# Kernel optimization log

Hardware: AMD Instinct MI355X
Metric: run time of the kernel (lower is better)

The kernel has to match this reference:

```python
import jax, jax.numpy as jnp
import numpy as np
from jax import lax

B, T_ENC, T_DEC = 32, 256, 256
N_MEL = 80
MEM_D = 768
ATT_RNN = 1024
DEC_RNN = 1024
PRENET = 256
ATT_D = 128
NF = 32
K = 31
PAD = (K - 1) // 2


def setup_inputs() -> dict:
    key = jax.random.key(0)
    ks = jax.random.split(key, 20)
    def w(k, shape, fan_in):
        return jax.random.normal(k, shape, jnp.float32) / np.sqrt(fan_in).astype(np.float32)
    inp = {}
    inp['memory'] = jax.random.normal(ks[0], (B, T_ENC, MEM_D), jnp.float32)
    inp['decoder_inputs'] = jax.random.normal(ks[1], (T_DEC, B, N_MEL), jnp.float32)
    inp['mask'] = jnp.zeros((B, T_ENC), bool)
    inp['prenet_W1'] = w(ks[2], (PRENET, N_MEL), N_MEL)
    inp['prenet_W2'] = w(ks[3], (PRENET, PRENET), PRENET)
    att_in = PRENET + MEM_D
    inp['att_Wih'] = w(ks[4], (4 * ATT_RNN, att_in), att_in)
    inp['att_Whh'] = w(ks[5], (4 * ATT_RNN, ATT_RNN), ATT_RNN)
    inp['att_bih'] = jnp.zeros((4 * ATT_RNN,), jnp.float32)
    inp['att_bhh'] = jnp.zeros((4 * ATT_RNN,), jnp.float32)
    inp['query_W'] = w(ks[6], (ATT_D, ATT_RNN), ATT_RNN)
    inp['memory_W'] = w(ks[7], (ATT_D, MEM_D), MEM_D)
    inp['v_W'] = w(ks[8], (1, ATT_D), ATT_D)
    inp['loc_conv_W'] = w(ks[9], (NF, 2, K), 2 * K)
    inp['loc_dense_W'] = w(ks[10], (ATT_D, NF), NF)
    dec_in = ATT_RNN + MEM_D
    inp['dec_Wih'] = w(ks[11], (4 * DEC_RNN, dec_in), dec_in)
    inp['dec_Whh'] = w(ks[12], (4 * DEC_RNN, DEC_RNN), DEC_RNN)
    inp['dec_bih'] = jnp.zeros((4 * DEC_RNN,), jnp.float32)
    inp['dec_bhh'] = jnp.zeros((4 * DEC_RNN,), jnp.float32)
    proj_in = DEC_RNN + MEM_D
    inp['proj_W'] = w(ks[13], (N_MEL, proj_in), proj_in)
    inp['proj_b'] = jnp.zeros((N_MEL,), jnp.float32)
    inp['gate_W'] = w(ks[14], (1, proj_in), proj_in)
    inp['gate_b'] = jnp.zeros((1,), jnp.float32)
    return inp


def _lstm_cell(x, h, c, Wih, Whh, bih, bhh):
    gates = x @ Wih.T + h @ Whh.T + (bih + bhh)
    i, f, g, o = jnp.split(gates, 4, axis=-1)
    c2 = jax.nn.sigmoid(f) * c + jax.nn.sigmoid(i) * jnp.tanh(g)
    h2 = jax.nn.sigmoid(o) * jnp.tanh(c2)
    return h2, c2


def _decode(memory, decoder_inputs, mask, prenet_W1, prenet_W2,
            att_Wih, att_Whh, att_bih, att_bhh,
            query_W, memory_W, v_W, loc_conv_W, loc_dense_W,
            dec_Wih, dec_Whh, dec_bih, dec_bhh,
            proj_W, proj_b, gate_W, gate_b):
    # teacher forcing: inputs are [go_frame, target[:-1]]
    go = jnp.zeros((1, B, N_MEL), decoder_inputs.dtype)
    x = jnp.concatenate([go, decoder_inputs[:-1]], axis=0)  # [T_DEC, B, N_MEL]
    # prenet (no dropout, p=0): two relu linears, bias=False
    x = jax.nn.relu(x @ prenet_W1.T)
    x = jax.nn.relu(x @ prenet_W2.T)  # [T_DEC, B, PRENET]
    processed_memory = memory @ memory_W.T  # [B, T_ENC, ATT_D]
    v = v_W[0]  # [ATT_D]

    def step(carry, x_t):
        att_h, att_c, dec_h, dec_c, aw, aw_cum, ctx = carry
        cell_in = jnp.concatenate([x_t, ctx], axis=-1)
        att_h, att_c = _lstm_cell(cell_in, att_h, att_c, att_Wih, att_Whh, att_bih, att_bhh)
        # location-sensitive attention
        awc = jnp.stack([aw, aw_cum], axis=1)  # [B, 2, T_ENC]
        loc = lax.conv_general_dilated(awc, loc_conv_W, window_strides=(1,),
                                       padding=[(PAD, PAD)],
                                       dimension_numbers=('NCH', 'OIH', 'NCH'))  # [B, NF, T_ENC]
        processed = jnp.einsum('bft,af->bta', loc, loc_dense_W)  # [B, T_ENC, ATT_D]
        query = att_h @ query_W.T  # [B, ATT_D]
        energies = jnp.einsum('bta,a->bt', jnp.tanh(processed + query[:, None, :] + processed_memory), v)
        energies = jnp.where(mask, -jnp.inf, energies)
        aw = jax.nn.softmax(energies, axis=1)  # [B, T_ENC]
        ctx = jnp.einsum('bt,btd->bd', aw, memory)  # [B, MEM_D]
        aw_cum = aw_cum + aw
        dec_in = jnp.concatenate([att_h, ctx], axis=-1)
        dec_h, dec_c = _lstm_cell(dec_in, dec_h, dec_c, dec_Wih, dec_Whh, dec_bih, dec_bhh)
        proj_in = jnp.concatenate([dec_h, ctx], axis=-1)
        mel = proj_in @ proj_W.T + proj_b  # [B, N_MEL]
        gate = (proj_in @ gate_W.T + gate_b)[:, 0]  # [B]
        return (att_h, att_c, dec_h, dec_c, aw, aw_cum, ctx), (mel, gate, aw)

    f32 = memory.dtype
    carry0 = (jnp.zeros((B, ATT_RNN), f32), jnp.zeros((B, ATT_RNN), f32),
              jnp.zeros((B, DEC_RNN), f32), jnp.zeros((B, DEC_RNN), f32),
              jnp.zeros((B, T_ENC), f32), jnp.zeros((B, T_ENC), f32),
              jnp.zeros((B, MEM_D), f32))
    _, (mels, gates, aligns) = lax.scan(step, carry0, x)
    # [B, T_DEC, N_MEL], [B, T_DEC], [B, T_DEC, T_ENC]
    return mels.transpose(1, 0, 2), gates.T, aligns.transpose(1, 0, 2)


def reference(memory, decoder_inputs, mask, prenet_W1, prenet_W2,
              att_Wih, att_Whh, att_bih, att_bhh,
              query_W, memory_W, v_W, loc_conv_W, loc_dense_W,
              dec_Wih, dec_Whh, dec_bih, dec_bhh,
              proj_W, proj_b, gate_W, gate_b):
    return _decode(memory, decoder_inputs, mask, prenet_W1, prenet_W2,
                   att_Wih, att_Whh, att_bih, att_bhh,
                   query_W, memory_W, v_W, loc_conv_W, loc_dense_W,
                   dec_Wih, dec_Whh, dec_bih, dec_bhh,
                   proj_W, proj_b, gate_W, gate_b)
```

## Files before the change

### kernel.cpp

```cpp
#include <hip/hip_runtime.h>
#include <cstddef>

#define TB   32
#define TENC 256
#define TDEC 256
#define NMEL 80
#define MEMD 768
#define ARNN 1024
#define PRN  256
#define ATTD 128
#define NFLT 32
#define KSZ  31
#define KPAD 15
#define SSTR 260
#define NAB  128
#define NEB  256
#define NCB  128
#define NATT 32

__device__ __forceinline__ float sigf(float x){ return 1.f/(1.f+expf(-x)); }

__global__ __launch_bounds__(256) void k_prenet1(const float* __restrict__ din,
                                                 const float* __restrict__ W1,
                                                 float* __restrict__ out){
  const int row = blockIdx.x;
  const int t = row >> 5, b = row & 31;
  const int tid = threadIdx.x;
  __shared__ float x[NMEL];
  if (tid < NMEL) x[tid] = (t == 0) ? 0.f : din[((size_t)(t-1)*TB + b)*NMEL + tid];
  __syncthreads();
  const float* wr = W1 + (size_t)tid*NMEL;
  float s = 0.f;
  #pragma unroll
  for (int m = 0; m < NMEL; ++m) s += x[m]*wr[m];
  out[(size_t)row*PRN + tid] = fmaxf(s, 0.f);
}

__global__ __launch_bounds__(256) void k_prenet2(float* __restrict__ buf,
                                                 const float* __restrict__ W2){
  const int row = blockIdx.x;
  const int tid = threadIdx.x;
  __shared__ float x[PRN];
  x[tid] = buf[(size_t)row*PRN + tid];
  __syncthreads();
  const float4* wr = (const float4*)(W2 + (size_t)tid*PRN);
  const float4* xx = (const float4*)x;
  float s = 0.f;
  #pragma unroll 8
  for (int k = 0; k < PRN/4; ++k) {
    float4 w = wr[k], v = xx[k];
    s += w.x*v.x + w.y*v.y + w.z*v.z + w.w*v.w;
  }
  buf[(size_t)row*PRN + tid] = fmaxf(s, 0.f);
}

__global__ __launch_bounds__(128) void k_procmem(const float* __restrict__ mem,
                                                 const float* __restrict__ mW,
                                                 float* __restrict__ pm){
  const int row = blockIdx.x;
  const int tid = threadIdx.x;
  __shared__ float x[MEMD];
  for (int i = tid; i < MEMD; i += 128) x[i] = mem[(size_t)row*MEMD + i];
  __syncthreads();
  const float4* wr = (const float4*)(mW + (size_t)tid*MEMD);
  const float4* xx = (const float4*)x;
  float s = 0.f;
  #pragma unroll 8
  for (int k = 0; k < MEMD/4; ++k) {
    float4 w = wr[k], v = xx[k];
    s += w.x*v.x + w.y*v.y + w.z*v.z + w.w*v.w;
  }
  pm[(size_t)row*ATTD + tid] = s;
}

__device__ __forceinline__ void lstm_body(int bi, int tid,
    float* smem, float* ldsg,
    const float* __restrict__ in1, int L1,
    const float* __restrict__ in2, int L2,
    const float* __restrict__ hbm,
    const float* __restrict__ Wih, const float* __restrict__ Whh,
    const float* __restrict__ bih, const float* __restrict__ bhh,
    const float* __restrict__ cT_in, float* cT_out, float* h_bm_out)
{
  const int Kin = L1 + L2, Ktot = Kin + ARNN;
  const int w = tid >> 6, lane = tid & 63;
  const int r = lane >> 4, kl = lane & 15;
  const int up = w >> 1, bh = w & 1, b0 = bh*16;
  const int j0 = bi*8 + up*4;
  float acc[4][16];
  #pragma unroll
  for (int u = 0; u < 4; ++u)
    #pragma unroll
    for (int b = 0; b < 16; ++b) acc[u][b] = 0.f;

  for (int kc = 0; kc < Ktot; kc += 256) {
    const float* src; int kq, Ls;
    if (kc < L1)       { src = in1; kq = kc;       Ls = L1; }
    else if (kc < Kin) { src = in2; kq = kc - L1;  Ls = L2; }
    else               { src = hbm; kq = kc - Kin; Ls = ARNN; }
    const float* Wb; int rs, kof;
    if (kc < Kin) { Wb = Wih; rs = Kin;  kof = kc; }
    else          { Wb = Whh; rs = ARNN; kof = kc - Kin; }
    float4 wv[4][4];
    {
      const float* wr0 = Wb + (size_t)(r*ARNN + j0)*rs + kof;
      #pragma unroll
      for (int u = 0; u < 4; ++u) {
        const float* wru = wr0 + (size_t)u*rs;
        wv[u][0] = *(const float4*)(wru + (0*16 + kl)*4);
        wv[u][1] = *(const float4*)(wru + (1*16 + kl)*4);
        wv[u][2] = *(const float4*)(wru + (2*16 + kl)*4);
        wv[u][3] = *(const float4*)(wru + (3*16 + kl)*4);
      }
    }
    __syncthreads();
    #pragma unroll
    for (int tc = 0; tc < 8; ++tc) {
      const int f4 = tid + tc*256;
      const int bb = f4 >> 6, k4 = f4 & 63;
      *(float4*)(&smem[bb*SSTR + k4*4]) =
          *(const float4*)(src + (size_t)bb*Ls + kq + k4*4);
    }
    __syncthreads();
    #pragma unroll
    for (int b = 0; b < 16; ++b) {
      const float* sb = &smem[(b0 + b)*SSTR + kl*4];
      const float4 s0 = *(const float4*)(sb + 0*64);
      const float4 s1 = *(const float4*)(sb + 1*64);
      const float4 s2 = *(const float4*)(sb + 2*64);
      const float4 s3 = *(const float4*)(sb + 3*64);
      #pragma unroll
      for (int u = 0; u < 4; ++u) {
        float a = acc[u][b];
        a = fmaf(wv[u][0].x,s0.x, fmaf(wv[u][0].y,s0.y, fmaf(wv[u][0].z,s0.z, fmaf(wv[u][0].w,s0.w, a))));
        a = fmaf(wv[u][1].x,s1.x, fmaf(wv[u][1].y,s1.y, fmaf(wv[u][1].z,s1.z, fmaf(wv[u][1].w,s1.w, a))));
        a = fmaf(wv[u][2].x,s2.x, fmaf(wv[u][2].y,s2.y, fmaf(wv[u][2].z,s2.z, fmaf(wv[u][2].w,s2.w, a))));
        a = fmaf(wv[u][3].x,s3.x, fmaf(wv[u][3].y,s3.y, fmaf(wv[u][3].z,s3.z, fmaf(wv[u][3].w,s3.w, a))));
        acc[u][b] = a;
      }
    }
  }
  #pragma unroll
  for (int u = 0; u < 4; ++u)
    #pragma unroll
    for (int b = 0; b < 16; ++b) {
      acc[u][b] += __shfl_xor(acc[u][b], 1);
      acc[u][b] += __shfl_xor(acc[u][b], 2);
      acc[u][b] += __shfl_xor(acc[u][b], 4);
      acc[u][b] += __shfl_xor(acc[u][b], 8);
    }
  if (kl == 0) {
    #pragma unroll
    for (int u = 0; u < 4; ++u)
      #pragma unroll
      for (int b = 0; b < 16; ++b)
        ldsg[((w*4 + u)*4 + r)*17 + b] = acc[u][b];
  }
  {
    const int u2 = lane >> 4, bl = lane & 15;
    const int b = b0 + bl, j = j0 + u2;
    const float gi = ldsg[((w*4 + u2)*4 + 0)*17 + bl] + bih[j]          + bhh[j];
    const float gf = ldsg[((w*4 + u2)*4 + 1)*17 + bl] + bih[ARNN + j]   + bhh[ARNN + j];
    const float gg = ldsg[((w*4 + u2)*4 + 2)*17 + bl] + bih[2*ARNN + j] + bhh[2*ARNN + j];
    const float go = ldsg[((w*4 + u2)*4 + 3)*17 + bl] + bih[3*ARNN + j] + bhh[3*ARNN + j];
    const float c  = sigf(gf)*cT_in[j*32 + b] + sigf(gi)*tanhf(gg);
    const float h  = sigf(go)*tanhf(c);
    cT_out[j*32 + b] = c;
    h_bm_out[(size_t)b*ARNN + j] = h;
  }
}

__device__ __forceinline__ void eterm_body(int eb, int tid, float* smem,
    const float* __restrict__ aw_prev, int awp_stride,
    const float* __restrict__ aw_cum,
    const float* __restrict__ conv_W, const float* __restrict__ dense_W,
    const float* __restrict__ pm, float* __restrict__ eterm)
{
  const int b   = eb >> 3;
  const int te0 = (eb & 7)*32;
  float* awp = smem;
  float* awc = smem + 64;
  float* cw  = smem + 128;
  float* loc = smem + 2112;
  if (tid < 62) {
    const int te = te0 - KPAD + tid;
    const bool ok = (te >= 0) && (te < TENC);
    awp[tid] = ok ? aw_prev[(size_t)b*awp_stride + te] : 0.f;
    awc[tid] = ok ? aw_cum[(size_t)b*TENC + te] : 0.f;
  }
  for (int i = tid; i < NFLT*2*KSZ; i += 256) cw[i] = conv_W[i];
  __syncthreads();
  {
    const int te = tid & 31;
    const int fq = tid >> 5;
    #pragma unroll
    for (int ff = 0; ff < 4; ++ff) {
      const int f = fq*4 + ff;
      const float* wf = cw + f*2*KSZ;
      float s = 0.f;
      #pragma unroll
      for (int kk = 0; kk < KSZ; ++kk) s += awp[te+kk]*wf[kk];
      #pragma unroll
      for (int kk = 0; kk < KSZ; ++kk) s += awc[te+kk]*wf[KSZ+kk];
      loc[f*33 + te] = s;
    }
  }
  __syncthreads();
  {
    const int a  = tid & 127;
    const int th = tid >> 7;
    float la[NFLT];
    const float* lr = dense_W + (size_t)a*NFLT;
    #pragma unroll
    for (int f = 0; f < NFLT; ++f) la[f] = lr[f];
    #pragma unroll
    for (int t4 = 0; t4 < 16; ++t4) {
      const int tel = th*16 + t4;
      const int te = te0 + tel;
      float accv = pm[((size_t)b*TENC + te)*ATTD + a];
      #pragma unroll 8
      for (int f = 0; f < NFLT; ++f) accv = fmaf(la[f], loc[f*33 + tel], accv);
      eterm[((size_t)b*TENC + te)*ATTD + a] = accv;
    }
  }
}

__device__ __forceinline__ void attn_body(int b, int tid, float* smem, int t,
    const float* __restrict__ att_h, const float* __restrict__ query_W,
    const float* __restrict__ v_W, const float* __restrict__ eterm,
    float* __restrict__ out_al, float* __restrict__ aw_cum,
    const float* __restrict__ mem, float* __restrict__ ctx_out)
{
  float* hrow = smem;
  float* qp   = smem + 1024;
  float* q    = smem + 1280;
  float* vv   = smem + 1408;
  float* aws  = smem + 1536;
  float* red  = smem + 1792;
  ((float4*)hrow)[tid] = ((const float4*)(att_h + (size_t)b*ARNN))[tid];
  if (tid < ATTD) vv[tid] = v_W[tid];
  __syncthreads();
  {
    const int a = tid & 127, kh = tid >> 7;
    const float4* wr = (const float4*)(query_W + (size_t)a*ARNN + kh*512);
    const float4* xx = (const float4*)(hrow + kh*512);
    float s = 0.f;
    #pragma unroll 8
    for (int k = 0; k < 128; ++k) {
      float4 w = wr[k], x = xx[k];
      s += w.x*x.x + w.y*x.y + w.z*x.z + w.w*x.w;
    }
    qp[tid] = s;
  }
  __syncthreads();
  if (tid < ATTD) q[tid] = qp[tid] + qp[128 + tid];
  __syncthreads();
  float e = 0.f;
  {
    const float* etr = eterm + ((size_t)b*TENC + tid)*ATTD;
    #pragma unroll 8
    for (int a4 = 0; a4 < 32; ++a4) {
      float4 t4 = *(const float4*)(etr + a4*4);
      e += vv[a4*4+0]*tanhf(q[a4*4+0] + t4.x);
      e += vv[a4*4+1]*tanhf(q[a4*4+1] + t4.y);
      e += vv[a4*4+2]*tanhf(q[a4*4+2] + t4.z);
      e += vv[a4*4+3]*tanhf(q[a4*4+3] + t4.w);
    }
  }
  float m1 = e;
  #pragma unroll
  for (int d = 1; d < 64; d <<= 1) m1 = fmaxf(m1, __shfl_xor(m1, d, 64));
  if ((tid & 63) == 0) red[tid >> 6] = m1;
  __syncthreads();
  const float mx = fmaxf(fmaxf(red[0], red[1]), fmaxf(red[2], red[3]));
  const float p = expf(e - mx);
  float s1 = p;
  #pragma unroll
  for (int d = 1; d < 64; d <<= 1) s1 += __shfl_xor(s1, d, 64);
  if ((tid & 63) == 0) red[4 + (tid >> 6)] = s1;
  __syncthreads();
  const float sden = red[4] + red[5] + red[6] + red[7];
  const float aw = p / sden;
  out_al[(size_t)b*TDEC*TENC + (size_t)t*TENC + tid] = aw;
  aw_cum[(size_t)b*TENC + tid] += aw;
  aws[tid] = aw;
  __syncthreads();
  if (tid < 192) {
    const float* mc = mem + (size_t)b*TENC*MEMD + tid*4;
    float4 s4 = make_float4(0.f, 0.f, 0.f, 0.f);
    #pragma unroll 8
    for (int te = 0; te < 256; ++te) {
      float4 m4 = *(const float4*)(mc + (size_t)te*MEMD);
      const float a = aws[te];
      s4.x = fmaf(a, m4.x, s4.x); s4.y = fmaf(a, m4.y, s4.y);
      s4.z = fmaf(a, m4.z, s4.z); s4.w = fmaf(a, m4.w, s4.w);
    }
    *(float4*)(ctx_out + (size_t)b*MEMD + tid*4) = s4;
  }
}

__global__ __launch_bounds__(256, 2) void k_phase1(
    int tA, int ncb,
    float* cx, float* ahbm2, float* dhbm, float* dcT,
    const float* __restrict__ dWih, const float* __restrict__ dWhh,
    const float* __restrict__ dbih, const float* __restrict__ dbhh,
    float* out_al, float* awcum,
    const float* __restrict__ et,
    const float* __restrict__ qW, const float* __restrict__ vW,
    const float* __restrict__ mem)
{
  __shared__ float smem[32*SSTR];
  __shared__ float ldsg[4*4*4*17];
  int bi = blockIdx.x;
  const int tid = threadIdx.x;
  if (bi < ncb) {
    const int tD = tA - 1;
    const int curD = tD & 1, nxtD = curD ^ 1;
    lstm_body(bi, tid, smem, ldsg,
        ahbm2 + (size_t)nxtD*TB*ARNN, ARNN,
        cx + (size_t)(tD+1)*TB*MEMD, MEMD,
        dhbm + (size_t)tD*TB*ARNN,
        dWih, dWhh, dbih, dbhh,
        dcT + (size_t)curD*ARNN*TB, dcT + (size_t)nxtD*ARNN*TB,
        dhbm + (size_t)(tD+1)*TB*ARNN);
    return;
  }
  bi -= ncb;
  const int nxt = (tA & 1) ^ 1;
  attn_body(bi, tid, smem, tA,
      ahbm2 + (size_t)nxt*TB*ARNN, qW, vW, et,
      out_al, awcum, mem, cx + (size_t)(tA+1)*TB*MEMD);
}

__global__ __launch_bounds__(256, 2) void k_phase2(
    int tA, int nab,
    const float* __restrict__ xp, const float* __restrict__ cx,
    float* ahbm2, float* acT,
    const float* __restrict__ aWih, const float* __restrict__ aWhh,
    const float* __restrict__ abih, const float* __restrict__ abhh,
    const float* __restrict__ aw0, const float* __restrict__ out_al,
    const float* __restrict__ awcum,
    const float* __restrict__ cvW, const float* __restrict__ ldW,
    const float* __restrict__ pm, float* __restrict__ et)
{
  __shared__ float smem[32*SSTR];
  __shared__ float ldsg[4*4*4*17];
  int bi = blockIdx.x;
  const int tid = threadIdx.x;
  if (bi < nab) {
    const int cur = tA & 1, nxt = cur ^ 1;
    lstm_body(bi, tid, smem, ldsg,
        xp + (size_t)tA*TB*PRN, PRN,
        cx + (size_t)tA*TB*MEMD, MEMD,
        ahbm2 + (size_t)cur*TB*ARNN,
        aWih, aWhh, abih, abhh,
        acT + (size_t)cur*ARNN*TB, acT + (size_t)nxt*ARNN*TB,
        ahbm2 + (size_t)nxt*TB*ARNN);
    return;
  }
  bi -= nab;
  {
    const float* awprev = (tA == 0) ? aw0 : (out_al + (size_t)(tA-1)*TENC);
    const int awps = (tA == 0) ? TENC : TDEC*TENC;
    eterm_body(bi, tid, smem, awprev, awps, awcum, cvW, ldW, pm, et);
  }
}

__global__ __launch_bounds__(192) void k_proj(
    const float* __restrict__ dh_all,
    const float* __restrict__ cx_all,
    const float* __restrict__ proj_W,
    const float* __restrict__ proj_b,
    const float* __restrict__ gate_W,
    const float* __restrict__ gate_b,
    float* __restrict__ out_mel,
    float* __restrict__ out_gate)
{
  const int b = blockIdx.y;
  const int tid = threadIdx.x;
  __shared__ float pin[ARNN + MEMD];
  __shared__ float pp[192];
  for (int t0 = 0; t0 < 32; ++t0) {
    const int t = blockIdx.x*32 + t0;
    __syncthreads();
    for (int i = tid; i < 448; i += 192) {
      float4 v;
      if (i < 256) v = *(const float4*)(dh_all + ((size_t)(t+1)*TB + b)*ARNN + i*4);
      else         v = *(const float4*)(cx_all + ((size_t)(t+1)*TB + b)*MEMD + (i-256)*4);
      *(float4*)(&pin[i*4]) = v;
    }
    __syncthreads();
    if (tid < 160) {
      const int m = tid >> 1, kh = tid & 1;
      const float4* wr = (const float4*)(proj_W + (size_t)m*1792 + kh*896);
      const float4* xx = (const float4*)(pin + kh*896);
      float s = 0.f;
      #pragma unroll 8
      for (int k = 0; k < 224; ++k) {
        float4 w = wr[k], x = xx[k];
        s += w.x*x.x + w.y*x.y + w.z*x.z + w.w*x.w;
      }
      pp[tid] = s;
    } else if (tid == 160) {
      const float4* wr = (const float4*)gate_W;
      const float4* xx = (const float4*)pin;
      float s = 0.f;
      #pragma unroll 8
      for (int k = 0; k < 448; ++k) {
        float4 w = wr[k], x = xx[k];
        s += w.x*x.x + w.y*x.y + w.z*x.z + w.w*x.w;
      }
      out_gate[(size_t)b*TDEC + t] = s + gate_b[0];
    }
    __syncthreads();
    if (tid < NMEL) out_mel[((size_t)b*TDEC + t)*NMEL + tid] = pp[2*tid] + pp[2*tid+1] + proj_b[tid];
  }
}

extern "C" void kernel_launch(void* const* d_in, const int* in_sizes, int n_in,
                              void* d_out, int out_size, void* d_ws, size_t ws_size,
                              hipStream_t stream) {
  const float* mem  = (const float*)d_in[0];
  const float* din  = (const float*)d_in[1];
  const float* pW1  = (const float*)d_in[3];
  const float* pW2  = (const float*)d_in[4];
  const float* aWih = (const float*)d_in[5];
  const float* aWhh = (const float*)d_in[6];
  const float* abih = (const float*)d_in[7];
  const float* abhh = (const float*)d_in[8];
  const float* qW   = (const float*)d_in[9];
  const float* mW   = (const float*)d_in[10];
  const float* vW   = (const float*)d_in[11];
  const float* cvW  = (const float*)d_in[12];
  const float* ldW  = (const float*)d_in[13];
  const float* dWih = (const float*)d_in[14];
  const float* dWhh = (const float*)d_in[15];
  const float* dbih = (const float*)d_in[16];
  const float* dbhh = (const float*)d_in[17];
  const float* prW  = (const float*)d_in[18];
  const float* prb  = (const float*)d_in[19];
  const float* gW   = (const float*)d_in[20];
  const float* gb   = (const float*)d_in[21];

  float* ws = (float*)d_ws;
  size_t o = 0;
  float* xp    = ws + o; o += (size_t)TDEC*TB*PRN;
  float* pm    = ws + o; o += (size_t)TB*TENC*ATTD;
  float* et    = ws + o; o += (size_t)TB*TENC*ATTD;
  float* acT   = ws + o; o += (size_t)2*ARNN*TB;
  float* dcT   = ws + o; o += (size_t)2*ARNN*TB;
  float* ahbm2 = ws + o; o += (size_t)2*TB*ARNN;
  float* dhbm  = ws + o; o += (size_t)(TDEC+1)*TB*ARNN;
  float* cx    = ws + o; o += (size_t)(TDEC+2)*TB*MEMD;
  float* awcum = ws + o; o += (size_t)TB*TENC;
  float* aw0   = ws + o; o += (size_t)TB*TENC;
  if (ws_size < o*sizeof(float)) return;

  float* out_mel  = (float*)d_out;
  float* out_gate = out_mel + (size_t)TB*TDEC*NMEL;
  float* out_al   = out_gate + (size_t)TB*TDEC;

  (void)hipMemsetAsync(acT, 0, (size_t)2*ARNN*TB*sizeof(float), stream);
  (void)hipMemsetAsync(dcT, 0, (size_t)2*ARNN*TB*sizeof(float), stream);
  (void)hipMemsetAsync(ahbm2, 0, (size_t)2*TB*ARNN*sizeof(float), stream);
  (void)hipMemsetAsync(dhbm, 0, (size_t)TB*ARNN*sizeof(float), stream);
  (void)hipMemsetAsync(cx, 0, (size_t)TB*MEMD*sizeof(float), stream);
  (void)hipMemsetAsync(awcum, 0, (size_t)TB*TENC*sizeof(float), stream);
  (void)hipMemsetAsync(aw0, 0, (size_t)TB*TENC*sizeof(float), stream);

  k_prenet1<<<TDEC*TB, 256, 0, stream>>>(din, pW1, xp);
  k_prenet2<<<TDEC*TB, 256, 0, stream>>>(xp, pW2);
  k_procmem<<<TB*TENC, 128, 0, stream>>>(mem, mW, pm);

  k_phase2<<<NAB + NEB, 256, 0, stream>>>(
      0, NAB, xp, cx, ahbm2, acT,
      aWih, aWhh, abih, abhh,
      aw0, out_al, awcum, cvW, ldW, pm, et);

  for (int t = 0; t < TDEC; ++t) {
    const int ncb = (t > 0) ? NCB : 0;
    k_phase1<<<ncb + NATT, 256, 0, stream>>>(
        t, ncb, cx, ahbm2, dhbm, dcT,
        dWih, dWhh, dbih, dbhh,
        out_al, awcum, et, qW, vW, mem);
    if (t < TDEC - 1) {
      k_phase2<<<NAB + NEB, 256, 0, stream>>>(
          t + 1, NAB, xp, cx, ahbm2, acT,
          aWih, aWhh, abih, abhh,
          aw0, out_al, awcum, cvW, ldW, pm, et);
    }
  }
  k_phase1<<<NCB, 256, 0, stream>>>(
      TDEC, NCB, cx, ahbm2, dhbm, dcT,
      dWih, dWhh, dbih, dbhh,
      out_al, awcum, et, qW, vW, mem);

  k_proj<<<dim3(8, TB), 192, 0, stream>>>(dhbm, cx, prW, prb, gW, gb, out_mel, out_gate);
}
```

Before: 21.58 ms.

## Split LSTM gate GEMVs into partial sums computed alongside attention

Each LSTM's gate computation is split into two parts. The parts that depend only on already-available hidden states (att Whh·h, and dec Wih·att_h plus dec Whh·dec_h) are computed into global partial-gate buffers in the same launch as attention. The remaining context- and prenet-dependent parts are finished in the next launch. This moves weight-streaming work off the serial critical path and balances the two per-step launches, at the cost of extra global round-trips for the partial gates and a more intricate dependency schedule.

```diff
diff --git a/kernel.cpp b/kernel.cpp
--- a/kernel.cpp
+++ b/kernel.cpp
@@ -13,9 +13,8 @@
 #define KSZ  31
 #define KPAD 15
 #define SSTR 260
-#define NAB  128
+#define NAF  128
 #define NEB  256
-#define NCB  128
 #define NATT 32
 
 __device__ __forceinline__ float sigf(float x){ return 1.f/(1.f+expf(-x)); }
@@ -73,16 +72,71 @@
   pm[(size_t)row*ATTD + tid] = s;
 }
 
-__device__ __forceinline__ void lstm_body(int bi, int tid,
-    float* smem, float* ldsg,
-    const float* __restrict__ in1, int L1,
-    const float* __restrict__ in2, int L2,
-    const float* __restrict__ hbm,
-    const float* __restrict__ Wih, const float* __restrict__ Whh,
-    const float* __restrict__ bih, const float* __restrict__ bhh,
-    const float* __restrict__ cT_in, float* cT_out, float* h_bm_out)
-{
-  const int Kin = L1 + L2, Ktot = Kin + ARNN;
+__device__ __forceinline__ void lstm_chunk(int tid, int r, int kl, int b0, int j0,
+    float* smem, const float* src, int Ls, int kq,
+    const float* W, int rs, int kof, float acc[4][16])
+{
+  float4 wv[4][4];
+  {
+    const float* wr0 = W + (size_t)(r*ARNN + j0)*rs + kof + kq;
+    #pragma unroll
+    for (int u = 0; u < 4; ++u) {
+      const float* wru = wr0 + (size_t)u*rs;
+      wv[u][0] = *(const float4*)(wru + (0*16 + kl)*4);
+      wv[u][1] = *(const float4*)(wru + (1*16 + kl)*4);
+      wv[u][2] = *(const float4*)(wru + (2*16 + kl)*4);
+      wv[u][3] = *(const float4*)(wru + (3*16 + kl)*4);
+    }
+  }
+  __syncthreads();
+  #pragma unroll
+  for (int tc = 0; tc < 8; ++tc) {
+    const int f4 = tid + tc*256;
+    const int bb = f4 >> 6, k4 = f4 & 63;
+    *(float4*)(&smem[bb*SSTR + k4*4]) =
+        *(const float4*)(src + (size_t)bb*Ls + kq + k4*4);
+  }
+  __syncthreads();
+  #pragma unroll
+  for (int b = 0; b < 16; ++b) {
+    const float* sb = &smem[(b0 + b)*SSTR + kl*4];
+    const float4 s0 = *(const float4*)(sb + 0*64);
+    const float4 s1 = *(const float4*)(sb + 1*64);
+    const float4 s2 = *(const float4*)(sb + 2*64);
+    const float4 s3 = *(const float4*)(sb + 3*64);
+    #pragma unroll
+    for (int u = 0; u < 4; ++u) {
+      float a = acc[u][b];
+      a = fmaf(wv[u][0].x,s0.x, fmaf(wv[u][0].y,s0.y, fmaf(wv[u][0].z,s0.z, fmaf(wv[u][0].w,s0.w, a))));
+      a = fmaf(wv[u][1].x,s1.x, fmaf(wv[u][1].y,s1.y, fmaf(wv[u][1].z,s1.z, fmaf(wv[u][1].w,s1.w, a))));
+      a = fmaf(wv[u][2].x,s2.x, fmaf(wv[u][2].y,s2.y, fmaf(wv[u][2].z,s2.z, fmaf(wv[u][2].w,s2.w, a))));
+      a = fmaf(wv[u][3].x,s3.x, fmaf(wv[u][3].y,s3.y, fmaf(wv[u][3].z,s3.z, fmaf(wv[u][3].w,s3.w, a))));
+      acc[u][b] = a;
+    }
+  }
+}
+
+__device__ __forceinline__ void lstm_reduce(int kl, int w, float* ldsg, float acc[4][16])
+{
+  #pragma unroll
+  for (int u = 0; u < 4; ++u)
+    #pragma unroll
+    for (int b = 0; b < 16; ++b) {
+      acc[u][b] += __shfl_xor(acc[u][b], 1);
+      acc[u][b] += __shfl_xor(acc[u][b], 2);
+      acc[u][b] += __shfl_xor(acc[u][b], 4);
+      acc[u][b] += __shfl_xor(acc[u][b], 8);
+    }
+  if (kl == 0) {
+    const int r = 0; (void)r;
+  }
+}
+
+__device__ __forceinline__ void lstm_part1(int bi, int tid, float* smem, float* ldsg,
+    const float* srcA, int LsA, const float* WA, int rsA, int kofA, int nchA,
+    const float* srcB, int LsB, const float* WB, int rsB, int kofB, int nchB,
+    float* __restrict__ gpart)
+{
   const int w = tid >> 6, lane = tid & 63;
   const int r = lane >> 4, kl = lane & 15;
   const int up = w >> 1, bh = w & 1, b0 = bh*16;
@@ -92,18 +146,59 @@
   for (int u = 0; u < 4; ++u)
     #pragma unroll
     for (int b = 0; b < 16; ++b) acc[u][b] = 0.f;
-
+  for (int c = 0; c < nchA; ++c)
+    lstm_chunk(tid, r, kl, b0, j0, smem, srcA, LsA, c*256, WA, rsA, kofA, acc);
+  for (int c = 0; c < nchB; ++c)
+    lstm_chunk(tid, r, kl, b0, j0, smem, srcB, LsB, c*256, WB, rsB, kofB, acc);
+  #pragma unroll
+  for (int u = 0; u < 4; ++u)
+    #pragma unroll
+    for (int b = 0; b < 16; ++b) {
+      acc[u][b] += __shfl_xor(acc[u][b], 1);
+      acc[u][b] += __shfl_xor(acc[u][b], 2);
+      acc[u][b] += __shfl_xor(acc[u][b], 4);
+      acc[u][b] += __shfl_xor(acc[u][b], 8);
+    }
+  if (kl == 0) {
+    #pragma unroll
+    for (int u = 0; u < 4; ++u)
+      #pragma unroll
+      for (int b = 0; b < 16; ++b)
+        ldsg[((w*4 + u)*4 + r)*17 + b] = acc[u][b];
+  }
+  __syncthreads();
+  for (int i = tid; i < 1024; i += 256) {
+    const int rr = i >> 8, u8 = (i >> 5) & 7, b = i & 31;
+    const int upp = u8 >> 2, uu = u8 & 3, bh2 = b >> 4, bl2 = b & 15;
+    gpart[(size_t)(rr*ARNN + bi*8 + u8)*32 + b] =
+        ldsg[(((upp*2 + bh2)*4 + uu)*4 + rr)*17 + bl2];
+  }
+}
+
+__device__ __forceinline__ void lstm_part2(int bi, int tid, float* smem, float* ldsg,
+    const float* in1, int L1, const float* in2, int L2,
+    const float* W, int rs, int kofBase,
+    const float* __restrict__ gpart,
+    const float* __restrict__ bih, const float* __restrict__ bhh,
+    const float* __restrict__ cT_in, float* cT_out, float* h_bm_out)
+{
+  const int w = tid >> 6, lane = tid & 63;
+  const int r = lane >> 4, kl = lane & 15;
+  const int up = w >> 1, bh = w & 1, b0 = bh*16;
+  const int j0 = bi*8 + up*4;
+  const int Ktot = L1 + L2;
+  float acc[4][16];
+  #pragma unroll
+  for (int u = 0; u < 4; ++u)
+    #pragma unroll
+    for (int b = 0; b < 16; ++b) acc[u][b] = 0.f;
   for (int kc = 0; kc < Ktot; kc += 256) {
     const float* src; int kq, Ls;
-    if (kc < L1)       { src = in1; kq = kc;       Ls = L1; }
-    else if (kc < Kin) { src = in2; kq = kc - L1;  Ls = L2; }
-    else               { src = hbm; kq = kc - Kin; Ls = ARNN; }
-    const float* Wb; int rs, kof;
-    if (kc < Kin) { Wb = Wih; rs = Kin;  kof = kc; }
-    else          { Wb = Whh; rs = ARNN; kof = kc - Kin; }
+    if (kc < L1) { src = in1; kq = kc;      Ls = L1; }
+    else         { src = in2; kq = kc - L1; Ls = L2; }
     float4 wv[4][4];
     {
-      const float* wr0 = Wb + (size_t)(r*ARNN + j0)*rs + kof;
+      const float* wr0 = W + (size_t)(r*ARNN + j0)*rs + kofBase + kc;
       #pragma unroll
       for (int u = 0; u < 4; ++u) {
         const float* wru = wr0 + (size_t)u*rs;
@@ -159,10 +254,14 @@
   {
     const int u2 = lane >> 4, bl = lane & 15;
     const int b = b0 + bl, j = j0 + u2;
-    const float gi = ldsg[((w*4 + u2)*4 + 0)*17 + bl] + bih[j]          + bhh[j];
-    const float gf = ldsg[((w*4 + u2)*4 + 1)*17 + bl] + bih[ARNN + j]   + bhh[ARNN + j];
-    const float gg = ldsg[((w*4 + u2)*4 + 2)*17 + bl] + bih[2*ARNN + j] + bhh[2*ARNN + j];
-    const float go = ldsg[((w*4 + u2)*4 + 3)*17 + bl] + bih[3*ARNN + j] + bhh[3*ARNN + j];
+    const float g0 = ldsg[((w*4 + u2)*4 + 0)*17 + bl] + gpart[(size_t)(0*ARNN + j)*32 + b];
+    const float g1 = ldsg[((w*4 + u2)*4 + 1)*17 + bl] + gpart[(size_t)(1*ARNN + j)*32 + b];
+    const float g2 = ldsg[((w*4 + u2)*4 + 2)*17 + bl] + gpart[(size_t)(2*ARNN + j)*32 + b];
+    const float g3 = ldsg[((w*4 + u2)*4 + 3)*17 + bl] + gpart[(size_t)(3*ARNN + j)*32 + b];
+    const float gi = g0 + bih[j]          + bhh[j];
+    const float gf = g1 + bih[ARNN + j]   + bhh[ARNN + j];
+    const float gg = g2 + bih[2*ARNN + j] + bhh[2*ARNN + j];
+    const float go = g3 + bih[3*ARNN + j] + bhh[3*ARNN + j];
     const float c  = sigf(gf)*cT_in[j*32 + b] + sigf(gi)*tanhf(gg);
     const float h  = sigf(go)*tanhf(c);
     cT_out[j*32 + b] = c;
@@ -299,45 +398,51 @@
   }
 }
 
-__global__ __launch_bounds__(256, 2) void k_phase1(
-    int tA, int ncb,
-    float* cx, float* ahbm2, float* dhbm, float* dcT,
-    const float* __restrict__ dWih, const float* __restrict__ dWhh,
-    const float* __restrict__ dbih, const float* __restrict__ dbhh,
+__global__ __launch_bounds__(256, 2) void k_lb(
+    int t,
+    const float* __restrict__ ahbm, float* cx,
     float* out_al, float* awcum,
     const float* __restrict__ et,
     const float* __restrict__ qW, const float* __restrict__ vW,
-    const float* __restrict__ mem)
+    const float* __restrict__ mem,
+    const float* __restrict__ aWhh,
+    const float* __restrict__ dWih, const float* __restrict__ dWhh,
+    const float* __restrict__ dhbm_t,
+    float* __restrict__ gpartA, float* __restrict__ gpartC)
 {
   __shared__ float smem[32*SSTR];
   __shared__ float ldsg[4*4*4*17];
   int bi = blockIdx.x;
   const int tid = threadIdx.x;
-  if (bi < ncb) {
-    const int tD = tA - 1;
-    const int curD = tD & 1, nxtD = curD ^ 1;
-    lstm_body(bi, tid, smem, ldsg,
-        ahbm2 + (size_t)nxtD*TB*ARNN, ARNN,
-        cx + (size_t)(tD+1)*TB*MEMD, MEMD,
-        dhbm + (size_t)tD*TB*ARNN,
-        dWih, dWhh, dbih, dbhh,
-        dcT + (size_t)curD*ARNN*TB, dcT + (size_t)nxtD*ARNN*TB,
-        dhbm + (size_t)(tD+1)*TB*ARNN);
+  if (bi < NATT) {
+    attn_body(bi, tid, smem, t, ahbm, qW, vW, et,
+        out_al, awcum, mem, cx + (size_t)(t+1)*TB*MEMD);
     return;
   }
-  bi -= ncb;
-  const int nxt = (tA & 1) ^ 1;
-  attn_body(bi, tid, smem, tA,
-      ahbm2 + (size_t)nxt*TB*ARNN, qW, vW, et,
-      out_al, awcum, mem, cx + (size_t)(tA+1)*TB*MEMD);
-}
-
-__global__ __launch_bounds__(256, 2) void k_phase2(
-    int tA, int nab,
-    const float* __restrict__ xp, const float* __restrict__ cx,
-    float* ahbm2, float* acT,
-    const float* __restrict__ aWih, const float* __restrict__ aWhh,
+  bi -= NATT;
+  if (bi < NAF) {
+    lstm_part1(bi, tid, smem, ldsg,
+        ahbm, ARNN, aWhh, ARNN, 0, 4,
+        nullptr, 0, nullptr, 0, 0, 0,
+        gpartA);
+    return;
+  }
+  bi -= NAF;
+  lstm_part1(bi, tid, smem, ldsg,
+      ahbm, ARNN, dWih, 1792, 0, 4,
+      dhbm_t, ARNN, dWhh, ARNN, 0, 4,
+      gpartC);
+}
+
+__global__ __launch_bounds__(256, 2) void k_la(
+    int t, int naf, int neb,
+    const float* __restrict__ xp, float* cx,
+    float* ahbm, float* acT, float* dhbm, float* dcT,
+    const float* __restrict__ aWih,
     const float* __restrict__ abih, const float* __restrict__ abhh,
+    const float* __restrict__ dWih,
+    const float* __restrict__ dbih, const float* __restrict__ dbhh,
+    const float* __restrict__ gpartA, const float* __restrict__ gpartC,
     const float* __restrict__ aw0, const float* __restrict__ out_al,
     const float* __restrict__ awcum,
     const float* __restrict__ cvW, const float* __restrict__ ldW,
@@ -347,22 +452,35 @@
   __shared__ float ldsg[4*4*4*17];
   int bi = blockIdx.x;
   const int tid = threadIdx.x;
-  if (bi < nab) {
-    const int cur = tA & 1, nxt = cur ^ 1;
-    lstm_body(bi, tid, smem, ldsg,
-        xp + (size_t)tA*TB*PRN, PRN,
-        cx + (size_t)tA*TB*MEMD, MEMD,
-        ahbm2 + (size_t)cur*TB*ARNN,
-        aWih, aWhh, abih, abhh,
+  if (bi < naf) {
+    const int cur = t & 1, nxt = cur ^ 1;
+    lstm_part2(bi, tid, smem, ldsg,
+        xp + (size_t)t*TB*PRN, PRN,
+        cx + (size_t)t*TB*MEMD, MEMD,
+        aWih, 1024, 0,
+        gpartA, abih, abhh,
         acT + (size_t)cur*ARNN*TB, acT + (size_t)nxt*ARNN*TB,
-        ahbm2 + (size_t)nxt*TB*ARNN);
+        ahbm);
     return;
   }
-  bi -= nab;
+  bi -= naf;
+  if (bi < neb) {
+    const float* awprev = (t == 0) ? aw0 : (out_al + (size_t)(t-1)*TENC);
+    const int awps = (t == 0) ? TENC : TDEC*TENC;
+    eterm_body(bi, tid, smem, awprev, awps, awcum, cvW, ldW, pm, et);
+    return;
+  }
+  bi -= neb;
   {
-    const float* awprev = (tA == 0) ? aw0 : (out_al + (size_t)(tA-1)*TENC);
-    const int awps = (tA == 0) ? TENC : TDEC*TENC;
-    eterm_body(bi, tid, smem, awprev, awps, awcum, cvW, ldW, pm, et);
+    const int tD = t - 1;
+    const int curD = tD & 1, nxtD = curD ^ 1;
+    lstm_part2(bi, tid, smem, ldsg,
+        cx + (size_t)(tD+1)*TB*MEMD, MEMD,
+        nullptr, 0,
+        dWih, 1792, 1024,
+        gpartC, dbih, dbhh,
+        dcT + (size_t)curD*ARNN*TB, dcT + (size_t)nxtD*ARNN*TB,
+        dhbm + (size_t)(tD+1)*TB*ARNN);
   }
 }
 
@@ -449,11 +567,13 @@
   float* et    = ws + o; o += (size_t)TB*TENC*ATTD;
   float* acT   = ws + o; o += (size_t)2*ARNN*TB;
   float* dcT   = ws + o; o += (size_t)2*ARNN*TB;
-  float* ahbm2 = ws + o; o += (size_t)2*TB*ARNN;
+  float* ahbm  = ws + o; o += (size_t)TB*ARNN;
   float* dhbm  = ws + o; o += (size_t)(TDEC+1)*TB*ARNN;
   float* cx    = ws + o; o += (size_t)(TDEC+2)*TB*MEMD;
   float* awcum = ws + o; o += (size_t)TB*TENC;
   float* aw0   = ws + o; o += (size_t)TB*TENC;
+  float* gpartA= ws + o; o += (size_t)4*ARNN*TB;
+  float* gpartC= ws + o; o += (size_t)4*ARNN*TB;
   if (ws_size < o*sizeof(float)) return;
 
   float* out_mel  = (float*)d_out;
@@ -462,38 +582,37 @@
 
   (void)hipMemsetAsync(acT, 0, (size_t)2*ARNN*TB*sizeof(float), stream);
   (void)hipMemsetAsync(dcT, 0, (size_t)2*ARNN*TB*sizeof(float), stream);
-  (void)hipMemsetAsync(ahbm2, 0, (size_t)2*TB*ARNN*sizeof(float), stream);
   (void)hipMemsetAsync(dhbm, 0, (size_t)TB*ARNN*sizeof(float), stream);
   (void)hipMemsetAsync(cx, 0, (size_t)TB*MEMD*sizeof(float), stream);
   (void)hipMemsetAsync(awcum, 0, (size_t)TB*TENC*sizeof(float), stream);
   (void)hipMemsetAsync(aw0, 0, (size_t)TB*TENC*sizeof(float), stream);
+  (void)hipMemsetAsync(gpartA, 0, (size_t)4*ARNN*TB*sizeof(float), stream);
 
   k_prenet1<<<TDEC*TB, 256, 0, stream>>>(din, pW1, xp);
   k_prenet2<<<TDEC*TB, 256, 0, stream>>>(xp, pW2);
   k_procmem<<<TB*TENC, 128, 0, stream>>>(mem, mW, pm);
 
-  k_phase2<<<NAB + NEB, 256, 0, stream>>>(
-      0, NAB, xp, cx, ahbm2, acT,
-      aWih, aWhh, abih, abhh,
+  k_la<<<NAF + NEB, 256, 0, stream>>>(
+      0, NAF, NEB, xp, cx, ahbm, acT, dhbm, dcT,
+      aWih, abih, abhh, dWih, dbih, dbhh, gpartA, gpartC,
       aw0, out_al, awcum, cvW, ldW, pm, et);
 
   for (int t = 0; t < TDEC; ++t) {
-    const int ncb = (t > 0) ? NCB : 0;
-    k_phase1<<<ncb + NATT, 256, 0, stream>>>(
-        t, ncb, cx, ahbm2, dhbm, dcT,
-        dWih, dWhh, dbih, dbhh,
-        out_al, awcum, et, qW, vW, mem);
+    k_lb<<<NATT + NAF + NAF, 256, 0, stream>>>(
+        t, ahbm, cx, out_al, awcum, et, qW, vW, mem,
+        aWhh, dWih, dWhh, dhbm + (size_t)t*TB*ARNN,
+        gpartA, gpartC);
     if (t < TDEC - 1) {
-      k_phase2<<<NAB + NEB, 256, 0, stream>>>(
-          t + 1, NAB, xp, cx, ahbm2, acT,
-          aWih, aWhh, abih, abhh,
+      k_la<<<NAF + NEB + NAF, 256, 0, stream>>>(
+          t + 1, NAF, NEB, xp, cx, ahbm, acT, dhbm, dcT,
+          aWih, abih, abhh, dWih, dbih, dbhh, gpartA, gpartC,
           aw0, out_al, awcum, cvW, ldW, pm, et);
     }
   }
-  k_phase1<<<NCB, 256, 0, stream>>>(
-      TDEC, NCB, cx, ahbm2, dhbm, dcT,
-      dWih, dWhh, dbih, dbhh,
-      out_al, awcum, et, qW, vW, mem);
+  k_la<<<NAF, 256, 0, stream>>>(
+      TDEC, 0, 0, xp, cx, ahbm, acT, dhbm, dcT,
+      aWih, abih, abhh, dWih, dbih, dbhh, gpartA, gpartC,
+      aw0, out_al, awcum, cvW, ldW, pm, et);
 
   k_proj<<<dim3(8, TB), 192, 0, stream>>>(dhbm, cx, prW, prb, gW, gb, out_mel, out_gate);
 }
```

Result: slower. 24.79 ms (+14.9%).

## Store LSTM weights as bf16 and reschedule decoder LSTM alongside attention LSTM

Applied to the files above, without the earlier changes.

Each call repacks the four LSTM weight matrices into bf16 with round-to-nearest-even, in a k-interleaved layout, so every step streams half the weight bytes. The decoder LSTM for step t-1 now runs in the same launch as the attention LSTM and energy term for step t. The per-step projection moves into the attention launch, which lets the full history buffers shrink to double buffers. The cost is a repack pass on every call and a loss of weight precision, which may fail a tight tolerance.

```diff
diff --git a/kernel.cpp b/kernel.cpp
--- a/kernel.cpp
+++ b/kernel.cpp
@@ -13,12 +13,28 @@
 #define KSZ  31
 #define KPAD 15
 #define SSTR 260
-#define NAB  128
+#define NAF  128
 #define NEB  256
 #define NCB  128
 #define NATT 32
-
+#define NPRJ 32
+
+typedef unsigned short us8 __attribute__((ext_vector_type(8)));
+__device__ __forceinline__ float b2f(unsigned short u){ return __uint_as_float(((unsigned)u) << 16); }
 __device__ __forceinline__ float sigf(float x){ return 1.f/(1.f+expf(-x)); }
+
+__global__ __launch_bounds__(256) void k_repack(const float* __restrict__ src,
+                                                unsigned short* __restrict__ dst, int K){
+  const int row = blockIdx.x;
+  for (int k = threadIdx.x; k < K; k += 256) {
+    const int c = k >> 8, rem = k & 255;
+    const int q = rem >> 6, kli = rem & 63;
+    const int kl = kli >> 2, i = kli & 3;
+    const unsigned u = __float_as_uint(src[(size_t)row*K + k]);
+    const unsigned r = (u + 0x7FFFu + ((u >> 16) & 1u)) >> 16;
+    dst[(size_t)row*K + c*256 + kl*16 + q*4 + i] = (unsigned short)r;
+  }
+}
 
 __global__ __launch_bounds__(256) void k_prenet1(const float* __restrict__ din,
                                                  const float* __restrict__ W1,
@@ -78,7 +94,8 @@
     const float* __restrict__ in1, int L1,
     const float* __restrict__ in2, int L2,
     const float* __restrict__ hbm,
-    const float* __restrict__ Wih, const float* __restrict__ Whh,
+    const unsigned short* __restrict__ Wih16, int Kih,
+    const unsigned short* __restrict__ Whh16,
     const float* __restrict__ bih, const float* __restrict__ bhh,
     const float* __restrict__ cT_in, float* cT_out, float* h_bm_out)
 {
@@ -98,20 +115,15 @@
     if (kc < L1)       { src = in1; kq = kc;       Ls = L1; }
     else if (kc < Kin) { src = in2; kq = kc - L1;  Ls = L2; }
     else               { src = hbm; kq = kc - Kin; Ls = ARNN; }
-    const float* Wb; int rs, kof;
-    if (kc < Kin) { Wb = Wih; rs = Kin;  kof = kc; }
-    else          { Wb = Whh; rs = ARNN; kof = kc - Kin; }
-    float4 wv[4][4];
-    {
-      const float* wr0 = Wb + (size_t)(r*ARNN + j0)*rs + kof;
-      #pragma unroll
-      for (int u = 0; u < 4; ++u) {
-        const float* wru = wr0 + (size_t)u*rs;
-        wv[u][0] = *(const float4*)(wru + (0*16 + kl)*4);
-        wv[u][1] = *(const float4*)(wru + (1*16 + kl)*4);
-        wv[u][2] = *(const float4*)(wru + (2*16 + kl)*4);
-        wv[u][3] = *(const float4*)(wru + (3*16 + kl)*4);
-      }
+    const unsigned short* Wb; int K, kof;
+    if (kc < Kin) { Wb = Wih16; K = Kih;  kof = kc; }
+    else          { Wb = Whh16; K = ARNN; kof = kc - Kin; }
+    us8 lo[4], hi[4];
+    #pragma unroll
+    for (int u = 0; u < 4; ++u) {
+      const unsigned short* wp = Wb + (size_t)(r*ARNN + j0 + u)*K + kof + kl*16;
+      lo[u] = *(const us8*)wp;
+      hi[u] = *(const us8*)(wp + 8);
     }
     __syncthreads();
     #pragma unroll
@@ -122,6 +134,14 @@
           *(const float4*)(src + (size_t)bb*Ls + kq + k4*4);
     }
     __syncthreads();
+    float4 wv[4][4];
+    #pragma unroll
+    for (int u = 0; u < 4; ++u) {
+      wv[u][0] = make_float4(b2f(lo[u][0]), b2f(lo[u][1]), b2f(lo[u][2]), b2f(lo[u][3]));
+      wv[u][1] = make_float4(b2f(lo[u][4]), b2f(lo[u][5]), b2f(lo[u][6]), b2f(lo[u][7]));
+      wv[u][2] = make_float4(b2f(hi[u][0]), b2f(hi[u][1]), b2f(hi[u][2]), b2f(hi[u][3]));
+      wv[u][3] = make_float4(b2f(hi[u][4]), b2f(hi[u][5]), b2f(hi[u][6]), b2f(hi[u][7]));
+    }
     #pragma unroll
     for (int b = 0; b < 16; ++b) {
       const float* sb = &smem[(b0 + b)*SSTR + kl*4];
@@ -299,45 +319,88 @@
   }
 }
 
-__global__ __launch_bounds__(256, 2) void k_phase1(
-    int tA, int ncb,
-    float* cx, float* ahbm2, float* dhbm, float* dcT,
-    const float* __restrict__ dWih, const float* __restrict__ dWhh,
-    const float* __restrict__ dbih, const float* __restrict__ dbhh,
+__device__ __forceinline__ void proj_body(int b, int tid, float* smem, int tD,
+    const float* __restrict__ dh,
+    const float* __restrict__ cxs,
+    const float* __restrict__ proj_W, const float* __restrict__ proj_b,
+    const float* __restrict__ gate_W, const float* __restrict__ gate_b,
+    float* __restrict__ out_mel, float* __restrict__ out_gate)
+{
+  float* pin = smem;
+  float* pp  = smem + 1792;
+  for (int i = tid; i < 448; i += 256) {
+    float4 v;
+    if (i < 256) v = *(const float4*)(dh + (size_t)b*ARNN + i*4);
+    else         v = *(const float4*)(cxs + (size_t)b*MEMD + (i-256)*4);
+    *(float4*)(&pin[i*4]) = v;
+  }
+  __syncthreads();
+  if (tid < 160) {
+    const int m = tid >> 1, kh = tid & 1;
+    const float4* wr = (const float4*)(proj_W + (size_t)m*1792 + kh*896);
+    const float4* xx = (const float4*)(pin + kh*896);
+    float s = 0.f;
+    #pragma unroll 8
+    for (int k = 0; k < 224; ++k) {
+      float4 w = wr[k], x = xx[k];
+      s += w.x*x.x + w.y*x.y + w.z*x.z + w.w*x.w;
+    }
+    pp[tid] = s;
+  } else if (tid == 160) {
+    const float4* wr = (const float4*)gate_W;
+    const float4* xx = (const float4*)pin;
+    float s = 0.f;
+    #pragma unroll 8
+    for (int k = 0; k < 448; ++k) {
+      float4 w = wr[k], x = xx[k];
+      s += w.x*x.x + w.y*x.y + w.z*x.z + w.w*x.w;
+    }
+    out_gate[(size_t)b*TDEC + tD] = s + gate_b[0];
+  }
+  __syncthreads();
+  if (tid < NMEL) out_mel[((size_t)b*TDEC + tD)*NMEL + tid] = pp[2*tid] + pp[2*tid+1] + proj_b[tid];
+}
+
+__global__ __launch_bounds__(256) void k_lb(
+    int t, int natt, int nprj,
+    const float* __restrict__ ahbm2, float* cx2,
     float* out_al, float* awcum,
     const float* __restrict__ et,
     const float* __restrict__ qW, const float* __restrict__ vW,
-    const float* __restrict__ mem)
+    const float* __restrict__ mem,
+    const float* __restrict__ dhbm2,
+    const float* __restrict__ prW, const float* __restrict__ prb,
+    const float* __restrict__ gW, const float* __restrict__ gb,
+    float* out_mel, float* out_gate)
 {
-  __shared__ float smem[32*SSTR];
-  __shared__ float ldsg[4*4*4*17];
+  __shared__ float smem[2208];
   int bi = blockIdx.x;
   const int tid = threadIdx.x;
-  if (bi < ncb) {
-    const int tD = tA - 1;
-    const int curD = tD & 1, nxtD = curD ^ 1;
-    lstm_body(bi, tid, smem, ldsg,
-        ahbm2 + (size_t)nxtD*TB*ARNN, ARNN,
-        cx + (size_t)(tD+1)*TB*MEMD, MEMD,
-        dhbm + (size_t)tD*TB*ARNN,
-        dWih, dWhh, dbih, dbhh,
-        dcT + (size_t)curD*ARNN*TB, dcT + (size_t)nxtD*ARNN*TB,
-        dhbm + (size_t)(tD+1)*TB*ARNN);
+  if (bi < natt) {
+    const int s = t & 1;
+    attn_body(bi, tid, smem, t,
+        ahbm2 + (size_t)s*TB*ARNN, qW, vW, et,
+        out_al, awcum, mem, cx2 + (size_t)s*TB*MEMD);
     return;
   }
-  bi -= ncb;
-  const int nxt = (tA & 1) ^ 1;
-  attn_body(bi, tid, smem, tA,
-      ahbm2 + (size_t)nxt*TB*ARNN, qW, vW, et,
-      out_al, awcum, mem, cx + (size_t)(tA+1)*TB*MEMD);
-}
-
-__global__ __launch_bounds__(256, 2) void k_phase2(
-    int tA, int nab,
-    const float* __restrict__ xp, const float* __restrict__ cx,
-    float* ahbm2, float* acT,
-    const float* __restrict__ aWih, const float* __restrict__ aWhh,
+  bi -= natt;
+  if (bi < nprj) {
+    const int tD = t - 1;
+    const int s = tD & 1;
+    proj_body(bi, tid, smem, tD,
+        dhbm2 + (size_t)s*TB*ARNN, cx2 + (size_t)s*TB*MEMD,
+        prW, prb, gW, gb, out_mel, out_gate);
+  }
+}
+
+__global__ __launch_bounds__(256, 2) void k_step(
+    int tA, int naf, int neb,
+    const float* __restrict__ xp, float* cx2,
+    float* ahbm2, float* acT, float* dhbm2, float* dcT,
+    const unsigned short* __restrict__ aWih16, const unsigned short* __restrict__ aWhh16,
     const float* __restrict__ abih, const float* __restrict__ abhh,
+    const unsigned short* __restrict__ dWih16, const unsigned short* __restrict__ dWhh16,
+    const float* __restrict__ dbih, const float* __restrict__ dbhh,
     const float* __restrict__ aw0, const float* __restrict__ out_al,
     const float* __restrict__ awcum,
     const float* __restrict__ cvW, const float* __restrict__ ldW,
@@ -347,73 +410,35 @@
   __shared__ float ldsg[4*4*4*17];
   int bi = blockIdx.x;
   const int tid = threadIdx.x;
-  if (bi < nab) {
-    const int cur = tA & 1, nxt = cur ^ 1;
+  if (bi < naf) {
+    const int sp = (tA - 1) & 1, sc = tA & 1;
     lstm_body(bi, tid, smem, ldsg,
         xp + (size_t)tA*TB*PRN, PRN,
-        cx + (size_t)tA*TB*MEMD, MEMD,
-        ahbm2 + (size_t)cur*TB*ARNN,
-        aWih, aWhh, abih, abhh,
-        acT + (size_t)cur*ARNN*TB, acT + (size_t)nxt*ARNN*TB,
-        ahbm2 + (size_t)nxt*TB*ARNN);
+        cx2 + (size_t)sp*TB*MEMD, MEMD,
+        ahbm2 + (size_t)sp*TB*ARNN,
+        aWih16, 1024, aWhh16, abih, abhh,
+        acT + (size_t)sp*ARNN*TB, acT + (size_t)sc*ARNN*TB,
+        ahbm2 + (size_t)sc*TB*ARNN);
     return;
   }
-  bi -= nab;
-  {
+  bi -= naf;
+  if (bi < neb) {
     const float* awprev = (tA == 0) ? aw0 : (out_al + (size_t)(tA-1)*TENC);
     const int awps = (tA == 0) ? TENC : TDEC*TENC;
     eterm_body(bi, tid, smem, awprev, awps, awcum, cvW, ldW, pm, et);
-  }
-}
-
-__global__ __launch_bounds__(192) void k_proj(
-    const float* __restrict__ dh_all,
-    const float* __restrict__ cx_all,
-    const float* __restrict__ proj_W,
-    const float* __restrict__ proj_b,
-    const float* __restrict__ gate_W,
-    const float* __restrict__ gate_b,
-    float* __restrict__ out_mel,
-    float* __restrict__ out_gate)
-{
-  const int b = blockIdx.y;
-  const int tid = threadIdx.x;
-  __shared__ float pin[ARNN + MEMD];
-  __shared__ float pp[192];
-  for (int t0 = 0; t0 < 32; ++t0) {
-    const int t = blockIdx.x*32 + t0;
-    __syncthreads();
-    for (int i = tid; i < 448; i += 192) {
-      float4 v;
-      if (i < 256) v = *(const float4*)(dh_all + ((size_t)(t+1)*TB + b)*ARNN + i*4);
-      else         v = *(const float4*)(cx_all + ((size_t)(t+1)*TB + b)*MEMD + (i-256)*4);
-      *(float4*)(&pin[i*4]) = v;
-    }
-    __syncthreads();
-    if (tid < 160) {
-      const int m = tid >> 1, kh = tid & 1;
-      const float4* wr = (const float4*)(proj_W + (size_t)m*1792 + kh*896);
-      const float4* xx = (const float4*)(pin + kh*896);
-      float s = 0.f;
-      #pragma unroll 8
-      for (int k = 0; k < 224; ++k) {
-        float4 w = wr[k], x = xx[k];
-        s += w.x*x.x + w.y*x.y + w.z*x.z + w.w*x.w;
-      }
-      pp[tid] = s;
-    } else if (tid == 160) {
-      const float4* wr = (const float4*)gate_W;
-      const float4* xx = (const float4*)pin;
-      float s = 0.f;
-      #pragma unroll 8
-      for (int k = 0; k < 448; ++k) {
-        float4 w = wr[k], x = xx[k];
-        s += w.x*x.x + w.y*x.y + w.z*x.z + w.w*x.w;
-      }
-      out_gate[(size_t)b*TDEC + t] = s + gate_b[0];
-    }
-    __syncthreads();
-    if (tid < NMEL) out_mel[((size_t)b*TDEC + t)*NMEL + tid] = pp[2*tid] + pp[2*tid+1] + proj_b[tid];
+    return;
+  }
+  bi -= neb;
+  {
+    const int tC = tA - 1;
+    const int sp = (tC - 1) & 1, sc = tC & 1;
+    lstm_body(bi, tid, smem, ldsg,
+        ahbm2 + (size_t)sc*TB*ARNN, ARNN,
+        cx2 + (size_t)sc*TB*MEMD, MEMD,
+        dhbm2 + (size_t)sp*TB*ARNN,
+        dWih16, 1792, dWhh16, dbih, dbhh,
+        dcT + (size_t)sp*ARNN*TB, dcT + (size_t)sc*ARNN*TB,
+        dhbm2 + (size_t)sc*TB*ARNN);
   }
 }
 
@@ -450,10 +475,14 @@
   float* acT   = ws + o; o += (size_t)2*ARNN*TB;
   float* dcT   = ws + o; o += (size_t)2*ARNN*TB;
   float* ahbm2 = ws + o; o += (size_t)2*TB*ARNN;
-  float* dhbm  = ws + o; o += (size_t)(TDEC+1)*TB*ARNN;
-  float* cx    = ws + o; o += (size_t)(TDEC+2)*TB*MEMD;
+  float* dhbm2 = ws + o; o += (size_t)2*TB*ARNN;
+  float* cx2   = ws + o; o += (size_t)2*TB*MEMD;
   float* awcum = ws + o; o += (size_t)TB*TENC;
   float* aw0   = ws + o; o += (size_t)TB*TENC;
+  unsigned short* aWih16 = (unsigned short*)(ws + o); o += (size_t)4*ARNN*1024/2;
+  unsigned short* aWhh16 = (unsigned short*)(ws + o); o += (size_t)4*ARNN*1024/2;
+  unsigned short* dWih16 = (unsigned short*)(ws + o); o += (size_t)4*ARNN*1792/2;
+  unsigned short* dWhh16 = (unsigned short*)(ws + o); o += (size_t)4*ARNN*1024/2;
   if (ws_size < o*sizeof(float)) return;
 
   float* out_mel  = (float*)d_out;
@@ -463,37 +492,44 @@
   (void)hipMemsetAsync(acT, 0, (size_t)2*ARNN*TB*sizeof(float), stream);
   (void)hipMemsetAsync(dcT, 0, (size_t)2*ARNN*TB*sizeof(float), stream);
   (void)hipMemsetAsync(ahbm2, 0, (size_t)2*TB*ARNN*sizeof(float), stream);
-  (void)hipMemsetAsync(dhbm, 0, (size_t)TB*ARNN*sizeof(float), stream);
-  (void)hipMemsetAsync(cx, 0, (size_t)TB*MEMD*sizeof(float), stream);
+  (void)hipMemsetAsync(dhbm2, 0, (size_t)2*TB*ARNN*sizeof(float), stream);
+  (void)hipMemsetAsync(cx2, 0, (size_t)2*TB*MEMD*sizeof(float), stream);
   (void)hipMemsetAsync(awcum, 0, (size_t)TB*TENC*sizeof(float), stream);
   (void)hipMemsetAsync(aw0, 0, (size_t)TB*TENC*sizeof(float), stream);
+
+  k_repack<<<4*ARNN, 256, 0, stream>>>(aWih, aWih16, 1024);
+  k_repack<<<4*ARNN, 256, 0, stream>>>(aWhh, aWhh16, 1024);
+  k_repack<<<4*ARNN, 256, 0, stream>>>(dWih, dWih16, 1792);
+  k_repack<<<4*ARNN, 256, 0, stream>>>(dWhh, dWhh16, 1024);
 
   k_prenet1<<<TDEC*TB, 256, 0, stream>>>(din, pW1, xp);
   k_prenet2<<<TDEC*TB, 256, 0, stream>>>(xp, pW2);
   k_procmem<<<TB*TENC, 128, 0, stream>>>(mem, mW, pm);
 
-  k_phase2<<<NAB + NEB, 256, 0, stream>>>(
-      0, NAB, xp, cx, ahbm2, acT,
-      aWih, aWhh, abih, abhh,
+  k_step<<<NAF + NEB, 256, 0, stream>>>(
+      0, NAF, NEB, xp, cx2, ahbm2, acT, dhbm2, dcT,
+      aWih16, aWhh16, abih, abhh, dWih16, dWhh16, dbih, dbhh,
       aw0, out_al, awcum, cvW, ldW, pm, et);
 
   for (int t = 0; t < TDEC; ++t) {
-    const int ncb = (t > 0) ? NCB : 0;
-    k_phase1<<<ncb + NATT, 256, 0, stream>>>(
-        t, ncb, cx, ahbm2, dhbm, dcT,
-        dWih, dWhh, dbih, dbhh,
-        out_al, awcum, et, qW, vW, mem);
+    k_lb<<<NATT + ((t > 0) ? NPRJ : 0), 256, 0, stream>>>(
+        t, NATT, (t > 0) ? NPRJ : 0,
+        ahbm2, cx2, out_al, awcum, et, qW, vW, mem,
+        dhbm2, prW, prb, gW, gb, out_mel, out_gate);
     if (t < TDEC - 1) {
-      k_phase2<<<NAB + NEB, 256, 0, stream>>>(
-          t + 1, NAB, xp, cx, ahbm2, acT,
-          aWih, aWhh, abih, abhh,
+      k_step<<<NAF + NEB + NCB, 256, 0, stream>>>(
+          t + 1, NAF, NEB, xp, cx2, ahbm2, acT, dhbm2, dcT,
+          aWih16, aWhh16, abih, abhh, dWih16, dWhh16, dbih, dbhh,
           aw0, out_al, awcum, cvW, ldW, pm, et);
-    }
-  }
-  k_phase1<<<NCB, 256, 0, stream>>>(
-      TDEC, NCB, cx, ahbm2, dhbm, dcT,
-      dWih, dWhh, dbih, dbhh,
-      out_al, awcum, et, qW, vW, mem);
-
-  k_proj<<<dim3(8, TB), 192, 0, stream>>>(dhbm, cx, prW, prb, gW, gb, out_mel, out_gate);
-}
+    } else {
+      k_step<<<NCB, 256, 0, stream>>>(
+          TDEC, 0, 0, xp, cx2, ahbm2, acT, dhbm2, dcT,
+          aWih16, aWhh16, abih, abhh, dWih16, dWhh16, dbih, dbhh,
+          aw0, out_al, awcum, cvW, ldW, pm, et);
+    }
+  }
+  k_lb<<<NPRJ, 256, 0, stream>>>(
+      TDEC, 0, NPRJ,
+      ahbm2, cx2, out_al, awcum, et, qW, vW, mem,
+      dhbm2, prW, prb, gW, gb, out_mel, out_gate);
+}
```

Result: slower. 22.56 ms (+4.6%).
